# Kernel tuning notes

Measured on AMD Instinct MI355X. Metric: run time of the kernel, lower is better.

## Reference

```python
import jax, jax.numpy as jnp
import numpy as np
import math

B, H, S, D = 4, 8, 512, 64

def setup_inputs() -> dict:
    key = jax.random.key(0)
    k1, k2, k3, k4, k5 = jax.random.split(key, 5)
    return {
        "query": jax.random.normal(k1, (B, H, S, D), dtype=jnp.float32),
        "key": jax.random.normal(k2, (B, H, S, D), dtype=jnp.float32),
        "value": jax.random.normal(k3, (B, H, S, D), dtype=jnp.float32),
        "relem": jax.random.normal(k4, (B, S, S, D), dtype=jnp.float32),
        "mask": jax.random.randint(k5, (B, S), 0, 2, dtype=jnp.int32),
    }

def reference(query, key, value, relem, mask):
    d = query.shape[-1]
    # relscore[b,h,s,t] = sum_d q[b,h,s,d] * relem[b,s,t,d]
    relscore = jnp.einsum("bhsd,bstd->bhst", query, relem)
    scores = jnp.einsum("bhsd,bhtd->bhst", query, key)
    scores = (relscore + scores) / math.sqrt(d)
    # mask [B,S] -> [B,1,S,S] (broadcast of key mask over query positions)
    m = mask[:, None, None, :]  # repeat over query dim is a broadcast
    scores = jnp.where(m == 0, jnp.float32(-1e9), scores)
    p_attn = jax.nn.softmax(scores, axis=-1)
    ans1 = jnp.einsum("bhst,bhtd->bhsd", p_attn, value)
    ans2 = jnp.einsum("bhst,bstd->bhsd", p_attn, relem)
    return ans1 + ans2, p_attn
```

## Files before the change

### kernel.cpp

```cpp
#include <hip/hip_runtime.h>


typedef __attribute__((ext_vector_type(8))) short short8;
typedef __attribute__((ext_vector_type(4))) float f32x4;

#define MFMA16(a, b, c) __builtin_amdgcn_mfma_f32_16x16x32_bf16(a, b, c, 0, 0, 0)

__device__ __forceinline__ unsigned short f2bf(float x) {
  unsigned int u = __float_as_uint(x);
  u += 0x7fffu + ((u >> 16) & 1u);
  return (unsigned short)(u >> 16);
}
__device__ __forceinline__ float bf2f(unsigned int s) {
  return __uint_as_float(s << 16);
}
__device__ __forceinline__ short8 pack8(const float4& a, const float4& b) {
  short8 r;
  r[0] = (short)f2bf(a.x); r[1] = (short)f2bf(a.y);
  r[2] = (short)f2bf(a.z); r[3] = (short)f2bf(a.w);
  r[4] = (short)f2bf(b.x); r[5] = (short)f2bf(b.y);
  r[6] = (short)f2bf(b.z); r[7] = (short)f2bf(b.w);
  return r;
}
__device__ __forceinline__ int RLI(int t, int d) {
  return ((t << 6) | d) ^ ((((t & 7) ^ ((t >> 3) & 7))) << 3);
}
__device__ __forceinline__ int SBI(int h, int t) {
  return ((h << 9) | t) ^ ((h & 7) << 3);
}

__global__ __launch_bounds__(256, 4)
void qk_mfma(const float* __restrict__ Q, const float* __restrict__ K,
             float* __restrict__ skout) {
  const int bh   = blockIdx.x >> 6;
  const int tile = blockIdx.x & 63;
  const int s0 = (tile >> 3) << 6;
  const int t0 = (tile & 7) << 6;
  const int w    = threadIdx.x >> 6;
  const int lane = threadIdx.x & 63;
  const int rrow = lane & 15;
  const int kg   = lane >> 4;

  const float* Qb = Q + ((size_t)bh << 15);
  const float* Kb = K + ((size_t)bh << 15);

  const float* qp = Qb + (((s0 + (w << 4) + rrow) << 6) + (kg << 3));
  const short8 a0 = pack8(*reinterpret_cast<const float4*>(qp),
                          *reinterpret_cast<const float4*>(qp + 4));
  const short8 a1 = pack8(*reinterpret_cast<const float4*>(qp + 32),
                          *reinterpret_cast<const float4*>(qp + 36));

  float* outb = skout + ((size_t)bh << 18);

  float4 b0, b1, b2, b3;
  {
    const float* kp = Kb + (((t0 + rrow) << 6) + (kg << 3));
    b0 = *reinterpret_cast<const float4*>(kp);
    b1 = *reinterpret_cast<const float4*>(kp + 4);
    b2 = *reinterpret_cast<const float4*>(kp + 32);
    b3 = *reinterpret_cast<const float4*>(kp + 36);
  }
#pragma unroll
  for (int nt = 0; nt < 4; ++nt) {
    const short8 bb0 = pack8(b0, b1);
    const short8 bb1 = pack8(b2, b3);
    if (nt < 3) {
      const float* kp = Kb + (((t0 + ((nt + 1) << 4) + rrow) << 6) + (kg << 3));
      b0 = *reinterpret_cast<const float4*>(kp);
      b1 = *reinterpret_cast<const float4*>(kp + 4);
      b2 = *reinterpret_cast<const float4*>(kp + 32);
      b3 = *reinterpret_cast<const float4*>(kp + 36);
    }
    f32x4 c = {0.0f, 0.0f, 0.0f, 0.0f};
    c = MFMA16(a0, bb0, c);
    c = MFMA16(a1, bb1, c);
    const int tcol = t0 + (nt << 4) + rrow;
    const int srow = s0 + (w << 4) + (kg << 2);
#pragma unroll
    for (int r = 0; r < 4; ++r)
      outb[(size_t)(srow + r) * 512 + tcol] = c[r];
  }
}

__global__ __launch_bounds__(256, 2)
void attn_v7(const float* __restrict__ Q, const float* __restrict__ R,
             const int* __restrict__ Mk, float* __restrict__ ans,
             float* __restrict__ pout) {
  __shared__ __align__(16) unsigned short smem[8 * 512 + 512 * 64];
  unsigned short* Sb = smem;
  unsigned short* Rl = smem + 8 * 512;

  const int tid = threadIdx.x;
  const int b = blockIdx.x >> 9;
  const int s = blockIdx.x & 511;
  const int bh0 = b << 3;

  const float* Rg = R + ((size_t)((b << 9) + s) << 15);

  {
    const int c16 = tid & 15;
    const int r0  = tid >> 4;
#pragma unroll
    for (int pg = 0; pg < 4; ++pg) {
      float4 tmp[8];
#pragma unroll
      for (int j = 0; j < 8; ++j) {
        const int t = (((pg << 3) + j) << 4) + r0;
        tmp[j] = *reinterpret_cast<const float4*>(Rg + (t << 6) + (c16 << 2));
      }
#pragma unroll
      for (int j = 0; j < 8; ++j) {
        const int t = (((pg << 3) + j) << 4) + r0;
        unsigned short* dst = &Rl[RLI(t, c16 << 2)];
        dst[0] = f2bf(tmp[j].x); dst[1] = f2bf(tmp[j].y);
        dst[2] = f2bf(tmp[j].z); dst[3] = f2bf(tmp[j].w);
      }
    }
  }
  __syncthreads();

  const int lane = tid & 63;
  const int w    = tid >> 6;
  const int nn   = lane & 15;
  const int kg   = lane >> 4;

  {
    const int hq = nn & 7;
    const float* Qg = Q + ((size_t)(((bh0 + hq) << 9) + s) << 6);
    const short8 aq0 = pack8(*reinterpret_cast<const float4*>(Qg + (kg << 3)),
                             *reinterpret_cast<const float4*>(Qg + (kg << 3) + 4));
    const short8 aq1 = pack8(*reinterpret_cast<const float4*>(Qg + 32 + (kg << 3)),
                             *reinterpret_cast<const float4*>(Qg + 36 + (kg << 3)));

#pragma unroll
    for (int i = 0; i < 8; ++i) {
      const int t0 = ((w << 3) + i) << 4;
      const short8 bb0 = *reinterpret_cast<const short8*>(&Rl[RLI(t0 + nn, kg << 3)]);
      const short8 bb1 = *reinterpret_cast<const short8*>(&Rl[RLI(t0 + nn, 32 + (kg << 3))]);
      f32x4 c = {0.0f, 0.0f, 0.0f, 0.0f};
      c = MFMA16(aq0, bb0, c);
      c = MFMA16(aq1, bb1, c);
      if (kg < 2) {
#pragma unroll
        for (int r = 0; r < 4; ++r)
          Sb[SBI((kg << 2) + r, t0 + nn)] = f2bf(c[r]);
      }
    }
  }
  __syncthreads();

  {
    float bias[8];
#pragma unroll
    for (int k = 0; k < 8; ++k)
      bias[k] = Mk[(b << 9) + lane + (k << 6)] ? 0.0f : -1.0e9f;

#pragma unroll
    for (int rr = 0; rr < 2; ++rr) {
      const int h = (w << 1) + rr;
      float* po = pout + ((size_t)(bh0 + h) << 18) + ((size_t)s << 9);

      float v[8];
#pragma unroll
      for (int k = 0; k < 8; ++k) {
        const int t = lane + (k << 6);
        v[k] = (bf2f((unsigned int)Sb[SBI(h, t)]) + po[t]) * 0.125f + bias[k];
      }
      float m = v[0];
#pragma unroll
      for (int k = 1; k < 8; ++k) m = fmaxf(m, v[k]);
      m = fmaxf(m, __shfl_xor(m, 1));
      m = fmaxf(m, __shfl_xor(m, 2));
      m = fmaxf(m, __shfl_xor(m, 4));
      m = fmaxf(m, __shfl_xor(m, 8));
      m = fmaxf(m, __shfl_xor(m, 16));
      m = fmaxf(m, __shfl_xor(m, 32));

      float e[8], ss = 0.0f;
#pragma unroll
      for (int k = 0; k < 8; ++k) { e[k] = __expf(v[k] - m); ss += e[k]; }
      ss += __shfl_xor(ss, 1);
      ss += __shfl_xor(ss, 2);
      ss += __shfl_xor(ss, 4);
      ss += __shfl_xor(ss, 8);
      ss += __shfl_xor(ss, 16);
      ss += __shfl_xor(ss, 32);
      const float inv = 1.0f / ss;

#pragma unroll
      for (int k = 0; k < 8; ++k) {
        const float p = e[k] * inv;
        const int t = lane + (k << 6);
        po[t] = p;
        Sb[SBI(h, t)] = f2bf(p);
      }
    }
  }
  __syncthreads();

  {
    const int n0 = w << 4;
    f32x4 acc = {0.0f, 0.0f, 0.0f, 0.0f};
#pragma unroll
    for (int ks = 0; ks < 16; ++ks) {
      const int tb = (ks << 5) + (kg << 3);
      const short8 af = *reinterpret_cast<const short8*>(&Sb[SBI(nn, tb)]);
      short8 bf;
#pragma unroll
      for (int j = 0; j < 8; ++j)
        bf[j] = (short)Rl[RLI(tb + j, n0 + nn)];
      acc = MFMA16(af, bf, acc);
    }
    if (kg < 2) {
#pragma unroll
      for (int r = 0; r < 4; ++r) {
        const int h = (kg << 2) + r;
        ans[((size_t)(((bh0 + h) << 9) + s) << 6) + n0 + nn] = acc[r];
      }
    }
  }
}

__global__ __launch_bounds__(256, 2)
void pv_mfma(const float* __restrict__ V, const float* __restrict__ pout,
             float* __restrict__ ans) {
  __shared__ __align__(16) unsigned short Vl[512 * 64];

  const int tid = threadIdx.x;
  const int bh = blockIdx.x >> 3;
  const int s0 = (blockIdx.x & 7) << 6;

  const float* Vg = V + ((size_t)bh << 15);
  {
    const int c16 = tid & 15;
    const int r0  = tid >> 4;
#pragma unroll
    for (int pg = 0; pg < 4; ++pg) {
      float4 tmp[8];
#pragma unroll
      for (int j = 0; j < 8; ++j) {
        const int t = (((pg << 3) + j) << 4) + r0;
        tmp[j] = *reinterpret_cast<const float4*>(Vg + (t << 6) + (c16 << 2));
      }
#pragma unroll
      for (int j = 0; j < 8; ++j) {
        const int t = (((pg << 3) + j) << 4) + r0;
        unsigned short* dst = &Vl[RLI(t, c16 << 2)];
        dst[0] = f2bf(tmp[j].x); dst[1] = f2bf(tmp[j].y);
        dst[2] = f2bf(tmp[j].z); dst[3] = f2bf(tmp[j].w);
      }
    }
  }
  __syncthreads();

  const int lane = tid & 63;
  const int w    = tid >> 6;
  const int nn   = lane & 15;
  const int kg   = lane >> 4;
  const int srow = s0 + (w << 4) + nn;

  const float* Pg = pout + ((size_t)bh << 18) + ((size_t)srow << 9);

  f32x4 acc0 = {0.f, 0.f, 0.f, 0.f}, acc1 = acc0, acc2 = acc0, acc3 = acc0;

  float4 pa = *reinterpret_cast<const float4*>(Pg + (kg << 3));
  float4 pb = *reinterpret_cast<const float4*>(Pg + (kg << 3) + 4);
#pragma unroll
  for (int ks = 0; ks < 16; ++ks) {
    const short8 af = pack8(pa, pb);
    if (ks < 15) {
      pa = *reinterpret_cast<const float4*>(Pg + ((ks + 1) << 5) + (kg << 3));
      pb = *reinterpret_cast<const float4*>(Pg + ((ks + 1) << 5) + (kg << 3) + 4);
    }
    const int tb = (ks << 5) + (kg << 3);
    short8 b0, b1, b2, b3;
#pragma unroll
    for (int j = 0; j < 8; ++j) {
      b0[j] = (short)Vl[RLI(tb + j, nn)];
      b1[j] = (short)Vl[RLI(tb + j, 16 + nn)];
      b2[j] = (short)Vl[RLI(tb + j, 32 + nn)];
      b3[j] = (short)Vl[RLI(tb + j, 48 + nn)];
    }
    acc0 = MFMA16(af, b0, acc0);
    acc1 = MFMA16(af, b1, acc1);
    acc2 = MFMA16(af, b2, acc2);
    acc3 = MFMA16(af, b3, acc3);
  }

  {
    const int sb = s0 + (w << 4) + (kg << 2);
#pragma unroll
    for (int r = 0; r < 4; ++r) {
      float* ap = ans + ((size_t)bh << 15) + ((size_t)(sb + r) << 6) + nn;
      ap[0]  += acc0[r];
      ap[16] += acc1[r];
      ap[32] += acc2[r];
      ap[48] += acc3[r];
    }
  }
}

extern "C" void kernel_launch(void* const* d_in, const int* in_sizes, int n_in,
                              void* d_out, int out_size, void* d_ws, size_t ws_size,
                              hipStream_t stream) {
  const float* Q  = (const float*)d_in[0];
  const float* K  = (const float*)d_in[1];
  const float* V  = (const float*)d_in[2];
  const float* R  = (const float*)d_in[3];
  const int*   Mk = (const int*)d_in[4];
  float* ans  = (float*)d_out;
  float* pout = ans + (size_t)4 * 8 * 512 * 64;
  (void)d_ws; (void)ws_size; (void)in_sizes; (void)n_in; (void)out_size;

  hipLaunchKernelGGL(qk_mfma, dim3(2048), dim3(256), 0, stream, Q, K, pout);
  hipLaunchKernelGGL(attn_v7, dim3(2048), dim3(256), 0, stream,
                     Q, R, Mk, ans, pout);
  hipLaunchKernelGGL(pv_mfma, dim3(256), dim3(256), 0, stream, V, pout, ans);
}
```

Measured before the change: 113.7 us.

## Stage QK scores as bf16 in workspace and split PV work across more blocks

The QK kernel can now write its scores as bf16 into the workspace buffer, and the attention kernel reads them back from there when the workspace is large enough. This halves the intermediate traffic and means the attention kernel no longer reads and then overwrites the same pout buffer. The PV kernel now runs twice as many blocks, each covering 32 rows, with every wave handling half of the D columns. That adds parallelism but makes each block reload the full V tile into shared memory, so V staging is duplicated.

```diff
diff --git a/kernel.cpp b/kernel.cpp
--- a/kernel.cpp
+++ b/kernel.cpp
@@ -29,9 +29,10 @@
   return ((h << 9) | t) ^ ((h & 7) << 3);
 }
 
+template <bool WSK>
 __global__ __launch_bounds__(256, 4)
 void qk_mfma(const float* __restrict__ Q, const float* __restrict__ K,
-             float* __restrict__ skout) {
+             void* __restrict__ skout) {
   const int bh   = blockIdx.x >> 6;
   const int tile = blockIdx.x & 63;
   const int s0 = (tile >> 3) << 6;
@@ -49,8 +50,6 @@
                           *reinterpret_cast<const float4*>(qp + 4));
   const short8 a1 = pack8(*reinterpret_cast<const float4*>(qp + 32),
                           *reinterpret_cast<const float4*>(qp + 36));
-
-  float* outb = skout + ((size_t)bh << 18);
 
   float4 b0, b1, b2, b3;
   {
@@ -76,16 +75,25 @@
     c = MFMA16(a1, bb1, c);
     const int tcol = t0 + (nt << 4) + rrow;
     const int srow = s0 + (w << 4) + (kg << 2);
-#pragma unroll
-    for (int r = 0; r < 4; ++r)
-      outb[(size_t)(srow + r) * 512 + tcol] = c[r];
-  }
-}
-
+    if constexpr (WSK) {
+      unsigned short* ob = (unsigned short*)skout + ((size_t)bh << 18);
+#pragma unroll
+      for (int r = 0; r < 4; ++r)
+        ob[(size_t)(srow + r) * 512 + tcol] = f2bf(c[r]);
+    } else {
+      float* ob = (float*)skout + ((size_t)bh << 18);
+#pragma unroll
+      for (int r = 0; r < 4; ++r)
+        ob[(size_t)(srow + r) * 512 + tcol] = c[r];
+    }
+  }
+}
+
+template <bool WSK>
 __global__ __launch_bounds__(256, 2)
-void attn_v7(const float* __restrict__ Q, const float* __restrict__ R,
-             const int* __restrict__ Mk, float* __restrict__ ans,
-             float* __restrict__ pout) {
+void attn_v7k(const float* __restrict__ Q, const float* __restrict__ R,
+              const int* __restrict__ Mk, float* __restrict__ ans,
+              float* __restrict__ pout, const void* __restrict__ skin) {
   __shared__ __align__(16) unsigned short smem[8 * 512 + 512 * 64];
   unsigned short* Sb = smem;
   unsigned short* Rl = smem + 8 * 512;
@@ -159,12 +167,19 @@
     for (int rr = 0; rr < 2; ++rr) {
       const int h = (w << 1) + rr;
       float* po = pout + ((size_t)(bh0 + h) << 18) + ((size_t)s << 9);
+      const unsigned short* skw =
+          WSK ? (const unsigned short*)skin + ((size_t)(bh0 + h) << 18) + ((size_t)s << 9)
+              : nullptr;
+      const float* skf =
+          WSK ? nullptr
+              : (const float*)skin + ((size_t)(bh0 + h) << 18) + ((size_t)s << 9);
 
       float v[8];
 #pragma unroll
       for (int k = 0; k < 8; ++k) {
         const int t = lane + (k << 6);
-        v[k] = (bf2f((unsigned int)Sb[SBI(h, t)]) + po[t]) * 0.125f + bias[k];
+        const float skv = WSK ? bf2f((unsigned int)skw[t]) : skf[t];
+        v[k] = (bf2f((unsigned int)Sb[SBI(h, t)]) + skv) * 0.125f + bias[k];
       }
       float m = v[0];
 #pragma unroll
@@ -227,8 +242,8 @@
   __shared__ __align__(16) unsigned short Vl[512 * 64];
 
   const int tid = threadIdx.x;
-  const int bh = blockIdx.x >> 3;
-  const int s0 = (blockIdx.x & 7) << 6;
+  const int bh = blockIdx.x >> 4;
+  const int s0 = (blockIdx.x & 15) << 5;
 
   const float* Vg = V + ((size_t)bh << 15);
   {
@@ -257,11 +272,13 @@
   const int w    = tid >> 6;
   const int nn   = lane & 15;
   const int kg   = lane >> 4;
-  const int srow = s0 + (w << 4) + nn;
+  const int rw   = w & 1;
+  const int ch   = w >> 1;
+  const int srow = s0 + (rw << 4) + nn;
 
   const float* Pg = pout + ((size_t)bh << 18) + ((size_t)srow << 9);
 
-  f32x4 acc0 = {0.f, 0.f, 0.f, 0.f}, acc1 = acc0, acc2 = acc0, acc3 = acc0;
+  f32x4 acc0 = {0.f, 0.f, 0.f, 0.f}, acc1 = acc0;
 
   float4 pa = *reinterpret_cast<const float4*>(Pg + (kg << 3));
   float4 pb = *reinterpret_cast<const float4*>(Pg + (kg << 3) + 4);
@@ -273,29 +290,23 @@
       pb = *reinterpret_cast<const float4*>(Pg + ((ks + 1) << 5) + (kg << 3) + 4);
     }
     const int tb = (ks << 5) + (kg << 3);
-    short8 b0, b1, b2, b3;
+    short8 b0, b1;
 #pragma unroll
     for (int j = 0; j < 8; ++j) {
-      b0[j] = (short)Vl[RLI(tb + j, nn)];
-      b1[j] = (short)Vl[RLI(tb + j, 16 + nn)];
-      b2[j] = (short)Vl[RLI(tb + j, 32 + nn)];
-      b3[j] = (short)Vl[RLI(tb + j, 48 + nn)];
+      b0[j] = (short)Vl[RLI(tb + j, (ch << 5) + nn)];
+      b1[j] = (short)Vl[RLI(tb + j, (ch << 5) + 16 + nn)];
     }
     acc0 = MFMA16(af, b0, acc0);
     acc1 = MFMA16(af, b1, acc1);
-    acc2 = MFMA16(af, b2, acc2);
-    acc3 = MFMA16(af, b3, acc3);
-  }
-
-  {
-    const int sb = s0 + (w << 4) + (kg << 2);
+  }
+
+  {
+    const int sb = s0 + (rw << 4) + (kg << 2);
 #pragma unroll
     for (int r = 0; r < 4; ++r) {
-      float* ap = ans + ((size_t)bh << 15) + ((size_t)(sb + r) << 6) + nn;
+      float* ap = ans + ((size_t)bh << 15) + ((size_t)(sb + r) << 6) + (ch << 5) + nn;
       ap[0]  += acc0[r];
       ap[16] += acc1[r];
-      ap[32] += acc2[r];
-      ap[48] += acc3[r];
     }
   }
 }
@@ -310,10 +321,20 @@
   const int*   Mk = (const int*)d_in[4];
   float* ans  = (float*)d_out;
   float* pout = ans + (size_t)4 * 8 * 512 * 64;
-  (void)d_ws; (void)ws_size; (void)in_sizes; (void)n_in; (void)out_size;
-
-  hipLaunchKernelGGL(qk_mfma, dim3(2048), dim3(256), 0, stream, Q, K, pout);
-  hipLaunchKernelGGL(attn_v7, dim3(2048), dim3(256), 0, stream,
-                     Q, R, Mk, ans, pout);
-  hipLaunchKernelGGL(pv_mfma, dim3(256), dim3(256), 0, stream, V, pout, ans);
-}
+  (void)in_sizes; (void)n_in; (void)out_size;
+
+  const size_t sk_bf16_bytes = (size_t)4 * 8 * 512 * 512 * 2;
+
+  if (ws_size >= sk_bf16_bytes) {
+    hipLaunchKernelGGL((qk_mfma<true>), dim3(2048), dim3(256), 0, stream,
+                       Q, K, d_ws);
+    hipLaunchKernelGGL((attn_v7k<true>), dim3(2048), dim3(256), 0, stream,
+                       Q, R, Mk, ans, pout, d_ws);
+  } else {
+    hipLaunchKernelGGL((qk_mfma<false>), dim3(2048), dim3(256), 0, stream,
+                       Q, K, pout);
+    hipLaunchKernelGGL((attn_v7k<false>), dim3(2048), dim3(256), 0, stream,
+                       Q, R, Mk, ans, pout, pout);
+  }
+  hipLaunchKernelGGL(pv_mfma, dim3(512), dim3(256), 0, stream, V, pout, ans);
+}
```

Measured after the change: 113.9 us. Within noise of the previous version (+0.1%).
